# Optimization experiments

Measured on AMD Instinct MI355X. Metric: run time of the kernel, lower is better.

Reference implementation:

```python
import jax, jax.numpy as jnp
import numpy as np


def setup_inputs() -> dict:
    key = jax.random.key(0)
    k1, k2, k3, k4, k5 = jax.random.split(key, 5)
    B, IN_N, POSE = 32, 8192, 64
    M = 8                     # matrix_pose_dim = sqrt(64)
    NH, S2, HID = 32, 256, 256  # in_n/(img^2), img^2, hidden_dim
    OUT_N = 64
    return {
        "current_pose": jax.random.normal(k1, (B, IN_N, POSE), jnp.float32),
        "w_current": 0.02 * jax.random.normal(k2, (1, 1, IN_N, M, M), jnp.float32),
        "w_next": 0.02 * jax.random.normal(k3, (OUT_N, M, M), jnp.float32),
        "E_proj": 0.02 * jax.random.normal(k4, (NH, S2, HID), jnp.float32),
        "rel_embedd": jax.random.normal(k5, (1, 1, POSE), jnp.float32),
    }


def reference(current_pose, w_current, w_next, E_proj, rel_embedd):
    B, IN_N, POSE = current_pose.shape
    M = w_current.shape[-1]           # matrix_pose_dim
    NH, S2, HID = E_proj.shape        # heads, img*img, hidden_dim
    OUT_N = w_next.shape[0]

    # w_current: (1,1,IN_N,M,M) -> (1,IN_N,M,M); per-capsule pose-matrix multiply
    wc = w_current.reshape(IN_N, M, M)[None]
    cp = current_pose.reshape(B, IN_N, M, M)
    cp = jnp.matmul(cp, wc)                      # (B, IN_N, M, M)

    # raw reshape (row-major, matches torch .reshape) then Linformer projection
    cp = cp.reshape(B, POSE, NH, 1, S2)
    cp = jnp.matmul(cp, E_proj)                  # (B, POSE, NH, 1, HID)
    cp = cp[:, :, :, 0, :]                       # squeeze(3) -> (B, POSE, NH, HID)
    cp = cp.reshape(B, NH * HID, POSE)           # raw reshape as in torch

    # dots = softmax over out_n axis of a constant tensor == uniform 1/OUT_N.
    # einsum('bij,bje->bie') with uniform dots == mean over j, broadcast over i.
    pooled = jnp.sum(cp, axis=1, keepdims=True) / OUT_N   # (B, 1, POSE)
    npc = jnp.broadcast_to(pooled, (B, OUT_N, POSE))

    # add relative embedding (h_out = w_out = output_img_size = 1)
    npc = npc.reshape(B, OUT_N, 1, 1, POSE) + rel_embedd  # (B,OUT_N,1,1,POSE)
    npc = jnp.transpose(npc, (0, 2, 3, 1, 4)).reshape(B, OUT_N, POSE)

    # next-layer pose-matrix multiply
    npc = npc.reshape(B, OUT_N, M, M)
    npc = jnp.matmul(npc, w_next[None])           # (B, OUT_N, M, M)
    npc = npc.reshape(B, 1, 1, OUT_N, POSE)
    return npc[:, 0]                              # squeeze(1) -> (B,1,OUT_N,POSE)
```

## Files before the change

kernel.cpp:

```cpp
#include <hip/hip_runtime.h>
#include <hip/hip_bf16.h>


typedef short short8_t __attribute__((ext_vector_type(8)));
typedef float f32x4_t __attribute__((ext_vector_type(4)));

__device__ __forceinline__ short f2bf(float f) {
    union { float f; unsigned u; } v; v.f = f;
    unsigned r = v.u + 0x7FFFu + ((v.u >> 16) & 1u);
    return (short)(r >> 16);
}

__global__ void k_prep(const float* __restrict__ WC, short* __restrict__ WCf,
                       const float* __restrict__ E, float* __restrict__ F) {
    if (blockIdx.x < 256) {
        int t   = blockIdx.x * 256 + threadIdx.x;
        int l   = t & 63;
        int pc  = (t >> 6) & 15;
        int rp  = t >> 10;
        int lhi = l >> 4;
        int j   = l & 15;
        int row = (pc * 4 + lhi) * 128 + rp * 2 + (j >> 3);
        const float* src = WC + ((size_t)row << 6) + (j & 7);
        short8_t o;
        #pragma unroll
        for (int k = 0; k < 8; ++k) o[k] = f2bf(src[k * 8]);
        ((short8_t*)WCf)[t] = o;
    } else {
        int idx = ((blockIdx.x - 256) * 256 + threadIdx.x) * 4;
        int q   = idx & 63;
        int row = idx >> 6;
        int r   = row >> 6;
        int e   = row & 63;
        int nh  = r >> 2;
        int s2  = ((r & 3) << 6) + e;
        const float* base = E + (((size_t)nh * 256 + s2) << 8) + q;
        float4 s0 = *(const float4*)(base);
        float4 s1 = *(const float4*)(base + 64);
        float4 s2v = *(const float4*)(base + 128);
        float4 s3 = *(const float4*)(base + 192);
        float4 o;
        o.x = s0.x + s1.x + s2v.x + s3.x;
        o.y = s0.y + s1.y + s2v.y + s3.y;
        o.z = s0.z + s1.z + s2v.z + s3.z;
        o.w = s0.w + s1.w + s2v.w + s3.w;
        *(float4*)(F + idx) = o;
    }
}

__global__ void k_smat_mfma(const float* __restrict__ CP, const short* __restrict__ WCf,
                            float* __restrict__ S) {
    int b  = blockIdx.y;
    int w  = threadIdx.x >> 6;
    int l  = threadIdx.x & 63;
    int gx = blockIdx.x;
    int half = gx & 1;
    int rp = (gx >> 1) * 4 + w;
    int r0 = rp * 2;

    int i16   = l & 15;
    int r_sel = i16 >> 3;
    int m1    = i16 & 7;
    int lhi   = l >> 4;

    const float* cp_base = CP + ((size_t)b << 19) + ((size_t)(r0 + r_sel) << 6) + m1 * 8;
    const short8_t* wf   = (const short8_t*)WCf + (size_t)rp * 1024 + (half * 8) * 64 + l;

    f32x4_t acc = {0.f, 0.f, 0.f, 0.f};
    #pragma unroll
    for (int c = 0; c < 8; ++c) {
        int p = (half * 8 + c) * 4 + lhi;
        const float* a_ptr = cp_base + ((size_t)p << 13);
        float4 a0 = *(const float4*)(a_ptr);
        float4 a1 = *(const float4*)(a_ptr + 4);
        short8_t af;
        af[0] = f2bf(a0.x); af[1] = f2bf(a0.y); af[2] = f2bf(a0.z); af[3] = f2bf(a0.w);
        af[4] = f2bf(a1.x); af[5] = f2bf(a1.y); af[6] = f2bf(a1.z); af[7] = f2bf(a1.w);
        acc = __builtin_amdgcn_mfma_f32_16x16x32_bf16(af, wf[c * 64], acc, 0, 0, 0);
    }
    float* Sd = S + ((size_t)half << 18) + ((size_t)b << 13);
    int col = i16;
    #pragma unroll
    for (int v = 0; v < 4; ++v) {
        int row = lhi * 4 + v;
        if (row < 8 && col < 8)
            Sd[(r0 << 6) + row * 8 + col] = acc[v];
        else if (row >= 8 && col >= 8)
            Sd[((r0 + 1) << 6) + (row - 8) * 8 + (col - 8)] = acc[v];
    }
}

__global__ void k_pool(const float* __restrict__ S, const float* __restrict__ F,
                       float* __restrict__ P) {
    int chunk = blockIdx.x;
    int b     = blockIdx.y;
    int w = threadIdx.x >> 6;
    int l = threadIdx.x & 63;
    int g  = l >> 4;
    int ql = l & 15;
    int jbase = chunk * 512 + w * 128;
    const float* S0 = S + ((size_t)b << 13);
    const float* S1 = S0 + (1u << 18);

    f32x4_t acc = {0.f, 0.f, 0.f, 0.f};
    #pragma unroll 4
    for (int s = 0; s < 32; ++s) {
        int j = jbase + s * 4 + g;
        float sv = S0[j] + S1[j];
        float4 fv = *(const float4*)(F + ((size_t)j << 6) + ql * 4);
        acc[0] += sv * fv.x;
        acc[1] += sv * fv.y;
        acc[2] += sv * fv.z;
        acc[3] += sv * fv.w;
    }
    #pragma unroll
    for (int c = 0; c < 4; ++c) {
        acc[c] += __shfl_xor(acc[c], 16, 64);
        acc[c] += __shfl_xor(acc[c], 32, 64);
    }
    if (l < 16) {
        float4 o; o.x = acc[0]; o.y = acc[1]; o.z = acc[2]; o.w = acc[3];
        *(float4*)(P + ((size_t)((b * 16 + chunk) * 4 + w) << 6) + ql * 4) = o;
    }
}

__global__ void k_final(const float* __restrict__ P, const float* __restrict__ rel,
                        const float* __restrict__ WN, float* __restrict__ out) {
    int b  = blockIdx.x;
    int oc = blockIdx.y;
    int t  = threadIdx.x;
    __shared__ float pool_s[64];
    if (t < 64) {
        float s = 0.f;
        #pragma unroll
        for (int c = 0; c < 64; ++c) s += P[((size_t)(b * 64 + c) << 6) + t];
        pool_s[t] = s * (1.0f / 64.0f) + rel[t];
    }
    __syncthreads();
    #pragma unroll
    for (int idx = t; idx < 1024; idx += 256) {
        int o = oc * 16 + (idx >> 6);
        int e = idx & 63;
        int m1 = e >> 3, m2 = e & 7;
        float a = 0.f;
        #pragma unroll
        for (int k = 0; k < 8; ++k)
            a += pool_s[m1 * 8 + k] * WN[o * 64 + k * 8 + m2];
        out[((size_t)b << 12) + o * 64 + e] = a;
    }
}

extern "C" void kernel_launch(void* const* d_in, const int* in_sizes, int n_in,
                              void* d_out, int out_size, void* d_ws, size_t ws_size,
                              hipStream_t stream) {
    const float* current_pose = (const float*)d_in[0];
    const float* w_current    = (const float*)d_in[1];
    const float* w_next       = (const float*)d_in[2];
    const float* E_proj       = (const float*)d_in[3];
    const float* rel_embedd   = (const float*)d_in[4];
    float* out = (float*)d_out;

    char* ws = (char*)d_ws;
    float* F   = (float*)(ws);
    float* S   = (float*)(ws + (2u << 20));
    float* P   = (float*)(ws + (4u << 20));
    short* WCf = (short*)(ws + (5u << 20));

    k_prep<<<dim3(768), dim3(256), 0, stream>>>(w_current, WCf, E_proj, F);
    k_smat_mfma<<<dim3(32, 32), dim3(256), 0, stream>>>(current_pose, WCf, S);
    k_pool<<<dim3(16, 32), dim3(256), 0, stream>>>(S, F, P);
    k_final<<<dim3(32, 4), dim3(256), 0, stream>>>(P, rel_embedd, w_next, out);
}
```

Baseline: 30.75 us.

## Fuse pose-matrix MFMA and pooling into one kernel via LDS tile

Merges the MFMA pose-matrix kernel and the pooling kernel into one kernel. Each block keeps its 512-element S tile in shared memory and immediately dots it against the matching F rows, writing one partial per block. This removes the S global round trip and a kernel launch, and halves the partials that k_final reads. It also replaces scalar bf16 rounding with the packed v_cvt_pk_bf16_f32 instruction. In exchange, each block now adds two barriers and a strided F read.

```diff
diff --git a/kernel.cpp b/kernel.cpp
--- a/kernel.cpp
+++ b/kernel.cpp
@@ -4,11 +4,18 @@
 
 typedef short short8_t __attribute__((ext_vector_type(8)));
 typedef float f32x4_t __attribute__((ext_vector_type(4)));
+typedef int   int4_t  __attribute__((ext_vector_type(4)));
 
 __device__ __forceinline__ short f2bf(float f) {
     union { float f; unsigned u; } v; v.f = f;
     unsigned r = v.u + 0x7FFFu + ((v.u >> 16) & 1u);
     return (short)(r >> 16);
+}
+
+__device__ __forceinline__ int cvt_pk(float x, float y) {
+    int r;
+    asm("v_cvt_pk_bf16_f32 %0, %1, %2" : "=v"(r) : "v"(x), "v"(y));
+    return r;
 }
 
 __global__ void k_prep(const float* __restrict__ WC, short* __restrict__ WCf,
@@ -48,20 +55,24 @@
     }
 }
 
-__global__ void k_smat_mfma(const float* __restrict__ CP, const short* __restrict__ WCf,
-                            float* __restrict__ S) {
-    int b  = blockIdx.y;
-    int w  = threadIdx.x >> 6;
-    int l  = threadIdx.x & 63;
-    int gx = blockIdx.x;
+__global__ void k_bc(const float* __restrict__ CP, const short* __restrict__ WCf,
+                     const float* __restrict__ F, float* __restrict__ P) {
+    int b    = blockIdx.y;
+    int gx   = blockIdx.x;
     int half = gx & 1;
-    int rp = (gx >> 1) * 4 + w;
+    int rpg  = gx >> 1;
+    int w = threadIdx.x >> 6;
+    int l = threadIdx.x & 63;
+    int rp = rpg * 4 + w;
     int r0 = rp * 2;
 
     int i16   = l & 15;
     int r_sel = i16 >> 3;
     int m1    = i16 & 7;
     int lhi   = l >> 4;
+
+    __shared__ float Stile[512];
+    __shared__ float red[4][64];
 
     const float* cp_base = CP + ((size_t)b << 19) + ((size_t)(r0 + r_sel) << 6) + m1 * 8;
     const short8_t* wf   = (const short8_t*)WCf + (size_t)rp * 1024 + (half * 8) * 64 + l;
@@ -73,55 +84,43 @@
         const float* a_ptr = cp_base + ((size_t)p << 13);
         float4 a0 = *(const float4*)(a_ptr);
         float4 a1 = *(const float4*)(a_ptr + 4);
-        short8_t af;
-        af[0] = f2bf(a0.x); af[1] = f2bf(a0.y); af[2] = f2bf(a0.z); af[3] = f2bf(a0.w);
-        af[4] = f2bf(a1.x); af[5] = f2bf(a1.y); af[6] = f2bf(a1.z); af[7] = f2bf(a1.w);
-        acc = __builtin_amdgcn_mfma_f32_16x16x32_bf16(af, wf[c * 64], acc, 0, 0, 0);
+        int4_t ai;
+        ai[0] = cvt_pk(a0.x, a0.y);
+        ai[1] = cvt_pk(a0.z, a0.w);
+        ai[2] = cvt_pk(a1.x, a1.y);
+        ai[3] = cvt_pk(a1.z, a1.w);
+        acc = __builtin_amdgcn_mfma_f32_16x16x32_bf16(
+            __builtin_bit_cast(short8_t, ai), wf[c * 64], acc, 0, 0, 0);
     }
-    float* Sd = S + ((size_t)half << 18) + ((size_t)b << 13);
     int col = i16;
     #pragma unroll
     for (int v = 0; v < 4; ++v) {
         int row = lhi * 4 + v;
         if (row < 8 && col < 8)
-            Sd[(r0 << 6) + row * 8 + col] = acc[v];
+            Stile[(w * 2 + 0) * 64 + row * 8 + col] = acc[v];
         else if (row >= 8 && col >= 8)
-            Sd[((r0 + 1) << 6) + (row - 8) * 8 + (col - 8)] = acc[v];
+            Stile[(w * 2 + 1) * 64 + (row - 8) * 8 + (col - 8)] = acc[v];
     }
-}
+    __syncthreads();
 
-__global__ void k_pool(const float* __restrict__ S, const float* __restrict__ F,
-                       float* __restrict__ P) {
-    int chunk = blockIdx.x;
-    int b     = blockIdx.y;
-    int w = threadIdx.x >> 6;
-    int l = threadIdx.x & 63;
-    int g  = l >> 4;
-    int ql = l & 15;
-    int jbase = chunk * 512 + w * 128;
-    const float* S0 = S + ((size_t)b << 13);
-    const float* S1 = S0 + (1u << 18);
-
-    f32x4_t acc = {0.f, 0.f, 0.f, 0.f};
-    #pragma unroll 4
-    for (int s = 0; s < 32; ++s) {
-        int j = jbase + s * 4 + g;
-        float sv = S0[j] + S1[j];
-        float4 fv = *(const float4*)(F + ((size_t)j << 6) + ql * 4);
-        acc[0] += sv * fv.x;
-        acc[1] += sv * fv.y;
-        acc[2] += sv * fv.z;
-        acc[3] += sv * fv.w;
+    int q  = threadIdx.x & 63;
+    int jg = threadIdx.x >> 6;
+    const float* Fb = F + (((size_t)rpg * 512 + jg * 128) << 6) + q;
+    const float* St = Stile + jg * 128;
+    float p0 = 0.f, p1 = 0.f, p2 = 0.f, p3 = 0.f;
+    #pragma unroll 8
+    for (int s = 0; s < 128; s += 4) {
+        p0 += St[s + 0] * Fb[(size_t)(s + 0) << 6];
+        p1 += St[s + 1] * Fb[(size_t)(s + 1) << 6];
+        p2 += St[s + 2] * Fb[(size_t)(s + 2) << 6];
+        p3 += St[s + 3] * Fb[(size_t)(s + 3) << 6];
     }
-    #pragma unroll
-    for (int c = 0; c < 4; ++c) {
-        acc[c] += __shfl_xor(acc[c], 16, 64);
-        acc[c] += __shfl_xor(acc[c], 32, 64);
-    }
-    if (l < 16) {
-        float4 o; o.x = acc[0]; o.y = acc[1]; o.z = acc[2]; o.w = acc[3];
-        *(float4*)(P + ((size_t)((b * 16 + chunk) * 4 + w) << 6) + ql * 4) = o;
-    }
+    red[jg][q] = (p0 + p1) + (p2 + p3);
+    __syncthreads();
+    if (threadIdx.x < 64)
+        P[((size_t)(b * 32 + gx) << 6) + threadIdx.x] =
+            red[0][threadIdx.x] + red[1][threadIdx.x] +
+            red[2][threadIdx.x] + red[3][threadIdx.x];
 }
 
 __global__ void k_final(const float* __restrict__ P, const float* __restrict__ rel,
@@ -133,7 +132,7 @@
     if (t < 64) {
         float s = 0.f;
         #pragma unroll
-        for (int c = 0; c < 64; ++c) s += P[((size_t)(b * 64 + c) << 6) + t];
+        for (int c = 0; c < 32; ++c) s += P[((size_t)(b * 32 + c) << 6) + t];
         pool_s[t] = s * (1.0f / 64.0f) + rel[t];
     }
     __syncthreads();
@@ -162,12 +161,10 @@
 
     char* ws = (char*)d_ws;
     float* F   = (float*)(ws);
-    float* S   = (float*)(ws + (2u << 20));
-    float* P   = (float*)(ws + (4u << 20));
-    short* WCf = (short*)(ws + (5u << 20));
+    short* WCf = (short*)(ws + (2u << 20));
+    float* P   = (float*)(ws + (3u << 20));
 
     k_prep<<<dim3(768), dim3(256), 0, stream>>>(w_current, WCf, E_proj, F);
-    k_smat_mfma<<<dim3(32, 32), dim3(256), 0, stream>>>(current_pose, WCf, S);
-    k_pool<<<dim3(16, 32), dim3(256), 0, stream>>>(S, F, P);
+    k_bc<<<dim3(32, 32), dim3(256), 0, stream>>>(current_pose, WCf, F, P);
     k_final<<<dim3(32, 4), dim3(256), 0, stream>>>(P, rel_embedd, w_next, out);
 }
```

Result: faster. 29.21 us (-5.0%).
